# Optimization experiments

Measured on AMD Instinct MI355X. Metric: run time of the kernel, lower is better.

Reference implementation:

```python
import jax, jax.numpy as jnp
import numpy as np

B, N, H, D = 4, 2048, 16, 64
FEATS = H * D  # 1024; module scales scores by sqrt(feats), not sqrt(head_dim)


def setup_inputs() -> dict:
    key = jax.random.key(0)
    ks = jax.random.split(key, 9)
    s = 1.0 / np.sqrt(D)
    return {
        "x": jax.random.normal(ks[0], (B, N, H, D), dtype=jnp.float32),
        "Wq": jax.random.uniform(ks[1], (H, D, D), jnp.float32, -s, s),
        "bq": jax.random.uniform(ks[2], (H, D), jnp.float32, -s, s),
        "Wk": jax.random.uniform(ks[3], (H, D, D), jnp.float32, -s, s),
        "bk": jax.random.uniform(ks[4], (H, D), jnp.float32, -s, s),
        "Wv": jax.random.uniform(ks[5], (H, D, D), jnp.float32, -s, s),
        "bv": jax.random.uniform(ks[6], (H, D), jnp.float32, -s, s),
        "Wo": jax.random.uniform(ks[7], (H, D, D), jnp.float32, -s, s),
        "bo": jax.random.uniform(ks[8], (H, D), jnp.float32, -s, s),
    }


def reference(x, Wq, bq, Wk, bk, Wv, bv, Wo, bo):
    # per-head linears as one batched einsum: [b,n,h,d] x [h,d,o] -> [b,n,h,o]
    q = jnp.einsum("bnhd,hdo->bnho", x, Wq) + bq
    k = jnp.einsum("bnhd,hdo->bnho", x, Wk) + bk
    v = jnp.einsum("bnhd,hdo->bnho", x, Wv) + bv
    sqrt_d = jnp.asarray(FEATS, x.dtype) ** 0.5  # sqrt(feats) per original code
    # scores: [b,h,i,j]
    score = jax.nn.softmax(jnp.einsum("bihf,bjhf->bhij", q, k) / sqrt_d, axis=-1)
    attn = jnp.einsum("bhij,bjhf->bihf", score, v)  # [b,n,h,d]
    out = jnp.einsum("bnhd,hdo->bnho", attn, Wo) + bo
    return out
```

## Files before the change

kernel.cpp:

```cpp
#include <hip/hip_runtime.h>

#define Bsz  4
#define Nseq 2048
#define Hn   16
#define Dh   64
#define BH   (Bsz*Hn)
#define NT   (Nseq/64)

#define AS1 __attribute__((address_space(1)))
#define AS3 __attribute__((address_space(3)))

typedef __attribute__((ext_vector_type(8))) short bf16x8;
typedef __attribute__((ext_vector_type(16))) float f32x16;
typedef __attribute__((ext_vector_type(4))) float f32x4;
typedef __attribute__((ext_vector_type(2))) float f32x2;

#define MFMA32 __builtin_amdgcn_mfma_f32_32x32x16_bf16

static __device__ __forceinline__ unsigned short f2bf(float f) {
    unsigned u = __float_as_uint(f);
    u = (u + 0x7fffu + ((u >> 16) & 1u)) >> 16;
    return (unsigned short)u;
}
static __device__ __forceinline__ float bf2f(unsigned short s) {
    return __uint_as_float((unsigned)s << 16);
}
static __device__ __forceinline__ unsigned cvt_pk_bf16(float lo, float hi) {
    unsigned r;
    asm("v_cvt_pk_bf16_f32 %0, %1, %2" : "=v"(r) : "v"(lo), "v"(hi));
    return r;
}
static __device__ __forceinline__ void swap32(unsigned &a, unsigned &b) {
    asm("v_permlane32_swap_b32 %0, %1" : "+v"(a), "+v"(b));
}
static __device__ __forceinline__ float exp2v(float x) {
    float r;
    asm("v_exp_f32 %0, %1" : "=v"(r) : "v"(x));
    return r;
}
static __device__ __forceinline__ f32x2 pk_add(f32x2 a, f32x2 b) {
    f32x2 d;
    asm("v_pk_add_f32 %0, %1, %2" : "=v"(d) : "v"(a), "v"(b));
    return d;
}

__global__ __launch_bounds__(256) void proj_kernel(
    const float* __restrict__ x,
    const float* __restrict__ Wq, const float* __restrict__ bq,
    const float* __restrict__ Wk, const float* __restrict__ bk,
    const float* __restrict__ Wv, const float* __restrict__ bv,
    unsigned short* __restrict__ gQ, unsigned short* __restrict__ gK,
    unsigned short* __restrict__ gVt)
{
    const int bh = blockIdx.x, h = bh & (Hn - 1), b = bh >> 4;
    const int n0 = blockIdx.y * 64;
    const int tid = threadIdx.x;
    const int w = tid >> 6, lane = tid & 63, l31 = lane & 31, l5 = lane >> 5;
    const int qi = w >> 1, oj = w & 1;

    const int nrow = n0 + qi * 32 + l31;
    const float* xrow = x + (((size_t)b * Nseq + nrow) * Hn + h) * Dh;

    bf16x8 xh[4], xl[4];
#pragma unroll
    for (int ks = 0; ks < 4; ++ks) {
        f32x4 v0 = *(const f32x4*)&xrow[ks * 16 + l5 * 8];
        f32x4 v1 = *(const f32x4*)&xrow[ks * 16 + l5 * 8 + 4];
#pragma unroll
        for (int e = 0; e < 4; ++e) {
            unsigned short h0 = f2bf(v0[e]);
            xh[ks][e] = (short)h0;
            xl[ks][e] = (short)f2bf(v0[e] - bf2f(h0));
            unsigned short h1 = f2bf(v1[e]);
            xh[ks][4 + e] = (short)h1;
            xl[ks][4 + e] = (short)f2bf(v1[e] - bf2f(h1));
        }
    }

    const int o = oj * 32 + l31;
    const float* Wm[3] = {Wq, Wk, Wv};

    f32x16 acc[3] = {};
#pragma unroll
    for (int m = 0; m < 3; ++m) {
        const float* Wb = Wm[m] + h * 4096 + o;
#pragma unroll
        for (int ks = 0; ks < 4; ++ks) {
            bf16x8 wh, wl;
#pragma unroll
            for (int e = 0; e < 8; ++e) {
                float wv = Wb[(ks * 16 + l5 * 8 + e) * 64];
                unsigned short hh = f2bf(wv);
                wh[e] = (short)hh;
                wl[e] = (short)f2bf(wv - bf2f(hh));
            }
            if (m < 2) {
                acc[m] = MFMA32(xh[ks], wh, acc[m], 0, 0, 0);
                acc[m] = MFMA32(xl[ks], wh, acc[m], 0, 0, 0);
                acc[m] = MFMA32(xh[ks], wl, acc[m], 0, 0, 0);
            } else {
                acc[2] = MFMA32(wh, xh[ks], acc[2], 0, 0, 0);
                acc[2] = MFMA32(wl, xh[ks], acc[2], 0, 0, 0);
                acc[2] = MFMA32(wh, xl[ks], acc[2], 0, 0, 0);
            }
        }
    }

    {
        float bias = bq[h * 64 + o];
#pragma unroll
        for (int r = 0; r < 16; ++r) {
            int nl = (r & 3) + 8 * (r >> 2) + 4 * l5;
            int n = n0 + qi * 32 + nl;
            gQ[((size_t)bh * Nseq + n) * Dh + o] =
                f2bf((acc[0][r] + bias) * 0.0450842200f);
        }
    }
    {
        float bias = bk[h * 64 + o];
#pragma unroll
        for (int r = 0; r < 16; ++r) {
            int nl = (r & 3) + 8 * (r >> 2) + 4 * l5;
            int n = n0 + qi * 32 + nl;
            int c = (((o >> 3) ^ (n & 7)) * 8) + (o & 7);
            gK[((size_t)bh * Nseq + n) * Dh + c] = f2bf(acc[1][r] + bias);
        }
    }
    {
#pragma unroll
        for (int r = 0; r < 16; ++r) {
            int ol = (r & 3) + 8 * (r >> 2) + 4 * l5;
            int ov = oj * 32 + ol;
            float bias = bv[h * 64 + ov];
            int nt = qi * 32 + l31;
            int c = (((nt >> 3) ^ (ov & 7)) * 8) + (nt & 7);
            gVt[(((size_t)bh * NT + (n0 >> 6)) * 64 + ov) * 64 + c] =
                f2bf(acc[2][r] + bias);
        }
    }
}

__global__ __launch_bounds__(256, 4) void flash_kernel(
    const unsigned short* __restrict__ gQ,
    const unsigned short* __restrict__ gK,
    const unsigned short* __restrict__ gVt,
    const float* __restrict__ Wo, const float* __restrict__ bo,
    float* __restrict__ out)
{
    __shared__ unsigned short kbuf[2][4096];
    __shared__ unsigned short vbuf[2][4096];

    const int bh = blockIdx.x, h = bh & (Hn - 1), b = bh >> 4;
    const int tid = threadIdx.x;
    const int w = tid >> 6, lane = tid & 63;
    const int l31 = lane & 31, l5 = lane >> 5;
    const int qrow = blockIdx.y * 128 + w * 32 + l31;

    bf16x8 qf[4];
#pragma unroll
    for (int kk = 0; kk < 4; ++kk)
        qf[kk] = *(const bf16x8*)&gQ[((size_t)bh * Nseq + qrow) * Dh + kk * 16 + l5 * 8];

    f32x16 acc[2] = {};
    float l = 0.f;

    auto stage_kv = [&](int t, int bufi) {
        const unsigned short* ks = gK + ((size_t)bh * Nseq + (size_t)t * 64) * Dh;
        const unsigned short* vs = gVt + ((size_t)(bh * NT + t)) * 4096;
#pragma unroll
        for (int i = 0; i < 2; ++i) {
            int off = w * 1024 + i * 512 + lane * 8;
            __builtin_amdgcn_global_load_lds((const AS1 void*)(ks + off),
                                             (AS3 void*)(&kbuf[bufi][w * 1024 + i * 512]), 16, 0, 0);
            __builtin_amdgcn_global_load_lds((const AS1 void*)(vs + off),
                                             (AS3 void*)(&vbuf[bufi][w * 1024 + i * 512]), 16, 0, 0);
        }
    };

    auto tile_step = [&](const unsigned short* __restrict__ kb,
                         const unsigned short* __restrict__ vb) {
        f32x16 s[2] = {};
#pragma unroll
        for (int nt = 0; nt < 2; ++nt) {
            const int row = nt * 32 + l31;
            const int roff = row * 64;
#pragma unroll
            for (int kk = 0; kk < 4; ++kk) {
                bf16x8 kf = *(const bf16x8*)&kb[roff + (((kk * 2 + l5) ^ (row & 7)) * 8)];
                s[nt] = MFMA32(kf, qf[kk], s[nt], 0, 0, 0);
            }
        }

#pragma unroll
        for (int nt = 0; nt < 2; ++nt)
#pragma unroll
            for (int r = 0; r < 16; ++r)
                s[nt][r] = exp2v(s[nt][r]);

        f32x2* sp0 = (f32x2*)&s[0];
        f32x2* sp1 = (f32x2*)&s[1];
        f32x2 u0 = pk_add(sp0[0], sp0[1]), u1 = pk_add(sp0[2], sp0[3]);
        f32x2 u2 = pk_add(sp0[4], sp0[5]), u3 = pk_add(sp0[6], sp0[7]);
        f32x2 u4 = pk_add(sp1[0], sp1[1]), u5 = pk_add(sp1[2], sp1[3]);
        f32x2 u6 = pk_add(sp1[4], sp1[5]), u7 = pk_add(sp1[6], sp1[7]);
        u0 = pk_add(u0, u1); u2 = pk_add(u2, u3);
        u4 = pk_add(u4, u5); u6 = pk_add(u6, u7);
        u0 = pk_add(u0, u2); u4 = pk_add(u4, u6);
        u0 = pk_add(u0, u4);
        l += u0[0] + u0[1];

#pragma unroll
        for (int ks = 0; ks < 4; ++ks) {
            const int nt = ks >> 1;
            const int b0 = 8 * (ks & 1);
            unsigned x0 = cvt_pk_bf16(s[nt][b0 + 0], s[nt][b0 + 1]);
            unsigned x1 = cvt_pk_bf16(s[nt][b0 + 2], s[nt][b0 + 3]);
            unsigned y0 = cvt_pk_bf16(s[nt][b0 + 4], s[nt][b0 + 5]);
            unsigned y1 = cvt_pk_bf16(s[nt][b0 + 6], s[nt][b0 + 7]);
            swap32(x0, y0);
            swap32(x1, y1);
            bf16x8 pf;
            ((unsigned*)&pf)[0] = x0; ((unsigned*)&pf)[1] = x1;
            ((unsigned*)&pf)[2] = y0; ((unsigned*)&pf)[3] = y1;
#pragma unroll
            for (int dt = 0; dt < 2; ++dt) {
                const int row = dt * 32 + l31;
                bf16x8 vf = *(const bf16x8*)&vb[row * 64 + (((ks * 2 + l5) ^ (row & 7)) * 8)];
                acc[dt] = MFMA32(vf, pf, acc[dt], 0, 0, 0);
            }
        }
    };

    stage_kv(0, 0);

#pragma unroll 1
    for (int t2 = 0; t2 < NT; t2 += 2) {
        __syncthreads();
        stage_kv(t2 + 1, 1);
        tile_step(kbuf[0], vbuf[0]);
        __syncthreads();
        if (t2 + 2 < NT) stage_kv(t2 + 2, 0);
        tile_step(kbuf[1], vbuf[1]);
    }

    __syncthreads();
    {
        unsigned short* wl = kbuf[0];
        for (int c = tid; c < 512; c += 256) {
            int o = c >> 3, c8 = c & 7;
            int cc = ((c8 ^ (o & 7)) * 8);
#pragma unroll
            for (int jj = 0; jj < 4; ++jj) wl[o * 64 + cc + jj]     = f2bf(Wo[(h * 64 + c8 * 8 + jj) * 64 + o]);
#pragma unroll
            for (int jj = 0; jj < 4; ++jj) wl[o * 64 + cc + 4 + jj] = f2bf(Wo[(h * 64 + c8 * 8 + 4 + jj) * 64 + o]);
        }
    }
    __syncthreads();

    l += __shfl_xor(l, 32);
    float inv = 1.f / l;
#pragma unroll
    for (int dt = 0; dt < 2; ++dt)
#pragma unroll
        for (int r = 0; r < 16; ++r) acc[dt][r] *= inv;

    const unsigned short* wot = kbuf[0];
    f32x16 oc[2] = {};
#pragma unroll
    for (int kk = 0; kk < 4; ++kk) {
        const int dt = kk >> 1;
        const int b0 = 8 * (kk & 1);
        unsigned x0 = cvt_pk_bf16(acc[dt][b0 + 0], acc[dt][b0 + 1]);
        unsigned x1 = cvt_pk_bf16(acc[dt][b0 + 2], acc[dt][b0 + 3]);
        unsigned y0 = cvt_pk_bf16(acc[dt][b0 + 4], acc[dt][b0 + 5]);
        unsigned y1 = cvt_pk_bf16(acc[dt][b0 + 6], acc[dt][b0 + 7]);
        swap32(x0, y0);
        swap32(x1, y1);
        bf16x8 af;
        ((unsigned*)&af)[0] = x0; ((unsigned*)&af)[1] = x1;
        ((unsigned*)&af)[2] = y0; ((unsigned*)&af)[3] = y1;
#pragma unroll
        for (int ot = 0; ot < 2; ++ot) {
            int row = ot * 32 + l31;
            bf16x8 wf = *(const bf16x8*)&wot[row * 64 + (((kk * 2 + l5) ^ (row & 7)) * 8)];
            oc[ot] = MFMA32(wf, af, oc[ot], 0, 0, 0);
        }
    }

    float* obase = out + (((size_t)b * Nseq + qrow) * Hn + h) * Dh;
#pragma unroll
    for (int ot = 0; ot < 2; ++ot)
#pragma unroll
        for (int rq = 0; rq < 4; ++rq) {
            int o = ot * 32 + rq * 8 + l5 * 4;
            f32x4 bb = *(const f32x4*)&bo[h * 64 + o];
            f32x4 vv;
            vv[0] = oc[ot][rq * 4 + 0] + bb[0];
            vv[1] = oc[ot][rq * 4 + 1] + bb[1];
            vv[2] = oc[ot][rq * 4 + 2] + bb[2];
            vv[3] = oc[ot][rq * 4 + 3] + bb[3];
            *(f32x4*)&obase[o] = vv;
        }
}

extern "C" void kernel_launch(void* const* d_in, const int* in_sizes, int n_in,
                              void* d_out, int out_size, void* d_ws, size_t ws_size,
                              hipStream_t stream) {
    const float* x  = (const float*)d_in[0];
    const float* Wq = (const float*)d_in[1];
    const float* bq = (const float*)d_in[2];
    const float* Wk = (const float*)d_in[3];
    const float* bk = (const float*)d_in[4];
    const float* Wv = (const float*)d_in[5];
    const float* bv = (const float*)d_in[6];
    const float* Wo = (const float*)d_in[7];
    const float* bo = (const float*)d_in[8];
    float* out = (float*)d_out;

    unsigned short* gQ  = (unsigned short*)d_ws;
    unsigned short* gK  = gQ + (size_t)BH * Nseq * Dh;
    unsigned short* gVt = gK + (size_t)BH * Nseq * Dh;

    proj_kernel<<<dim3(BH, Nseq / 64), 256, 0, stream>>>(x, Wq, bq, Wk, bk, Wv, bv, gQ, gK, gVt);
    flash_kernel<<<dim3(BH, Nseq / 128), 256, 0, stream>>>(gQ, gK, gVt, Wo, bo, out);
}
```

Measured before the change: 113.9 us.

## Pre-split projection weights and software-pipeline QK with softmax-PV over 32-key tiles

Adds a small kernel that transposes Wq/Wk/Wv and splits them into bf16 hi/lo halves once, so the projection kernel loads ready bf16x8 fragments instead of doing strided fp32 loads and conversions. The flash kernel moves from 64-key tiles to 32-key tiles, with a four-slot K ring and a two-slot V ring. The QK MFMA for the next tile is issued while the exp and PV of the current tile run, aiming to overlap matrix and transcendental work. The costs are an extra kernel launch, more barriers per key, and redundant clamped loads at the end of the loop.

Result: slower. 131.1 us (+15.1%).

```diff
diff --git a/kernel.cpp b/kernel.cpp
--- a/kernel.cpp
+++ b/kernel.cpp
@@ -5,7 +5,7 @@
 #define Hn   16
 #define Dh   64
 #define BH   (Bsz*Hn)
-#define NT   (Nseq/64)
+#define NT32 (Nseq/32)
 
 #define AS1 __attribute__((address_space(1)))
 #define AS3 __attribute__((address_space(3)))
@@ -14,6 +14,7 @@
 typedef __attribute__((ext_vector_type(16))) float f32x16;
 typedef __attribute__((ext_vector_type(4))) float f32x4;
 typedef __attribute__((ext_vector_type(2))) float f32x2;
+typedef __attribute__((ext_vector_type(4))) unsigned short u16x4;
 
 #define MFMA32 __builtin_amdgcn_mfma_f32_32x32x16_bf16
 
@@ -44,11 +45,45 @@
     return d;
 }
 
+__global__ __launch_bounds__(256) void wprep_kernel(
+    const float* __restrict__ Wq, const float* __restrict__ Wk,
+    const float* __restrict__ Wv,
+    unsigned short* __restrict__ gWtH, unsigned short* __restrict__ gWtL)
+{
+    __shared__ float ws[64][65];
+    const int mh = blockIdx.x;
+    const int m = mh >> 4, h = mh & 15;
+    const int tid = threadIdx.x;
+    const float* W = (m == 0 ? Wq : (m == 1 ? Wk : Wv)) + h * 4096;
+
+    for (int c = tid; c < 1024; c += 256) {
+        int row = c >> 4, col = (c & 15) * 4;
+        *(f32x4*)&ws[row][col] = *(const f32x4*)&W[row * 64 + col];
+    }
+    __syncthreads();
+
+    const int o = tid >> 2, dblk = (tid & 3) * 16;
+    size_t base = ((size_t)mh * 64 + o) * 64 + dblk;
+#pragma unroll
+    for (int i4 = 0; i4 < 4; ++i4) {
+        u16x4 vh, vl;
+#pragma unroll
+        for (int j = 0; j < 4; ++j) {
+            float v = ws[dblk + i4 * 4 + j][o];
+            unsigned short hh = f2bf(v);
+            vh[j] = hh;
+            vl[j] = f2bf(v - bf2f(hh));
+        }
+        *(u16x4*)&gWtH[base + i4 * 4] = vh;
+        *(u16x4*)&gWtL[base + i4 * 4] = vl;
+    }
+}
+
 __global__ __launch_bounds__(256) void proj_kernel(
     const float* __restrict__ x,
-    const float* __restrict__ Wq, const float* __restrict__ bq,
-    const float* __restrict__ Wk, const float* __restrict__ bk,
-    const float* __restrict__ Wv, const float* __restrict__ bv,
+    const unsigned short* __restrict__ gWtH, const unsigned short* __restrict__ gWtL,
+    const float* __restrict__ bq, const float* __restrict__ bk,
+    const float* __restrict__ bv,
     unsigned short* __restrict__ gQ, unsigned short* __restrict__ gK,
     unsigned short* __restrict__ gVt)
 {
@@ -78,22 +113,16 @@
     }
 
     const int o = oj * 32 + l31;
-    const float* Wm[3] = {Wq, Wk, Wv};
 
     f32x16 acc[3] = {};
 #pragma unroll
     for (int m = 0; m < 3; ++m) {
-        const float* Wb = Wm[m] + h * 4096 + o;
+        const unsigned short* WH = gWtH + (((size_t)m * 16 + h) * 64 + o) * 64;
+        const unsigned short* WL = gWtL + (((size_t)m * 16 + h) * 64 + o) * 64;
 #pragma unroll
         for (int ks = 0; ks < 4; ++ks) {
-            bf16x8 wh, wl;
-#pragma unroll
-            for (int e = 0; e < 8; ++e) {
-                float wv = Wb[(ks * 16 + l5 * 8 + e) * 64];
-                unsigned short hh = f2bf(wv);
-                wh[e] = (short)hh;
-                wl[e] = (short)f2bf(wv - bf2f(hh));
-            }
+            bf16x8 wh = *(const bf16x8*)&WH[ks * 16 + l5 * 8];
+            bf16x8 wl = *(const bf16x8*)&WL[ks * 16 + l5 * 8];
             if (m < 2) {
                 acc[m] = MFMA32(xh[ks], wh, acc[m], 0, 0, 0);
                 acc[m] = MFMA32(xl[ks], wh, acc[m], 0, 0, 0);
@@ -127,14 +156,15 @@
         }
     }
     {
+        const int tile = (n0 >> 5) + qi;
+        const int kt = l31;
 #pragma unroll
         for (int r = 0; r < 16; ++r) {
             int ol = (r & 3) + 8 * (r >> 2) + 4 * l5;
             int ov = oj * 32 + ol;
             float bias = bv[h * 64 + ov];
-            int nt = qi * 32 + l31;
-            int c = (((nt >> 3) ^ (ov & 7)) * 8) + (nt & 7);
-            gVt[(((size_t)bh * NT + (n0 >> 6)) * 64 + ov) * 64 + c] =
+            int c = (((kt >> 3) ^ ((ov >> 2) & 3)) * 8) + (kt & 7);
+            gVt[(((size_t)bh * NT32 + tile) * 64 + ov) * 32 + c] =
                 f2bf(acc[2][r] + bias);
         }
     }
@@ -147,8 +177,8 @@
     const float* __restrict__ Wo, const float* __restrict__ bo,
     float* __restrict__ out)
 {
-    __shared__ unsigned short kbuf[2][4096];
-    __shared__ unsigned short vbuf[2][4096];
+    __shared__ unsigned short kbuf[4][2048];
+    __shared__ unsigned short vbuf[2][2048];
 
     const int bh = blockIdx.x, h = bh & (Hn - 1), b = bh >> 4;
     const int tid = threadIdx.x;
@@ -161,62 +191,53 @@
     for (int kk = 0; kk < 4; ++kk)
         qf[kk] = *(const bf16x8*)&gQ[((size_t)bh * Nseq + qrow) * Dh + kk * 16 + l5 * 8];
 
+    float z0 = 0.f;
+    asm volatile("" : "+v"(z0));
+    f32x16 zc = {z0, z0, z0, z0, z0, z0, z0, z0, z0, z0, z0, z0, z0, z0, z0, z0};
+
     f32x16 acc[2] = {};
     float l = 0.f;
 
-    auto stage_kv = [&](int t, int bufi) {
-        const unsigned short* ks = gK + ((size_t)bh * Nseq + (size_t)t * 64) * Dh;
-        const unsigned short* vs = gVt + ((size_t)(bh * NT + t)) * 4096;
-#pragma unroll
-        for (int i = 0; i < 2; ++i) {
-            int off = w * 1024 + i * 512 + lane * 8;
-            __builtin_amdgcn_global_load_lds((const AS1 void*)(ks + off),
-                                             (AS3 void*)(&kbuf[bufi][w * 1024 + i * 512]), 16, 0, 0);
-            __builtin_amdgcn_global_load_lds((const AS1 void*)(vs + off),
-                                             (AS3 void*)(&vbuf[bufi][w * 1024 + i * 512]), 16, 0, 0);
-        }
+    auto stageK = [&](int t, int slot) {
+        const unsigned short* src = gK + ((size_t)bh * Nseq + (size_t)t * 32) * Dh + tid * 8;
+        __builtin_amdgcn_global_load_lds((const AS1 void*)src,
+                                         (AS3 void*)(&kbuf[slot][w * 512]), 16, 0, 0);
     };
-
-    auto tile_step = [&](const unsigned short* __restrict__ kb,
-                         const unsigned short* __restrict__ vb) {
-        f32x16 s[2] = {};
-#pragma unroll
-        for (int nt = 0; nt < 2; ++nt) {
-            const int row = nt * 32 + l31;
-            const int roff = row * 64;
-#pragma unroll
-            for (int kk = 0; kk < 4; ++kk) {
-                bf16x8 kf = *(const bf16x8*)&kb[roff + (((kk * 2 + l5) ^ (row & 7)) * 8)];
-                s[nt] = MFMA32(kf, qf[kk], s[nt], 0, 0, 0);
-            }
-        }
-
-#pragma unroll
-        for (int nt = 0; nt < 2; ++nt)
-#pragma unroll
-            for (int r = 0; r < 16; ++r)
-                s[nt][r] = exp2v(s[nt][r]);
-
-        f32x2* sp0 = (f32x2*)&s[0];
-        f32x2* sp1 = (f32x2*)&s[1];
-        f32x2 u0 = pk_add(sp0[0], sp0[1]), u1 = pk_add(sp0[2], sp0[3]);
-        f32x2 u2 = pk_add(sp0[4], sp0[5]), u3 = pk_add(sp0[6], sp0[7]);
-        f32x2 u4 = pk_add(sp1[0], sp1[1]), u5 = pk_add(sp1[2], sp1[3]);
-        f32x2 u6 = pk_add(sp1[4], sp1[5]), u7 = pk_add(sp1[6], sp1[7]);
+    auto stageV = [&](int t, int slot) {
+        const unsigned short* src = gVt + ((size_t)(bh * NT32 + t)) * 2048 + tid * 8;
+        __builtin_amdgcn_global_load_lds((const AS1 void*)src,
+                                         (AS3 void*)(&vbuf[slot][w * 512]), 16, 0, 0);
+    };
+
+    auto qk_tile = [&](const unsigned short* __restrict__ kb) -> f32x16 {
+        const int roff = l31 * 64;
+        const int sw = l31 & 7;
+        bf16x8 kf = *(const bf16x8*)&kb[roff + ((l5 ^ sw) * 8)];
+        f32x16 s = MFMA32(kf, qf[0], zc, 0, 0, 0);
+#pragma unroll
+        for (int kk = 1; kk < 4; ++kk) {
+            kf = *(const bf16x8*)&kb[roff + (((kk * 2 + l5) ^ sw) * 8)];
+            s = MFMA32(kf, qf[kk], s, 0, 0, 0);
+        }
+        return s;
+    };
+
+    auto soft_pv = [&](f32x16& s, const unsigned short* __restrict__ vb) {
+#pragma unroll
+        for (int r = 0; r < 16; ++r) s[r] = exp2v(s[r]);
+        f32x2* sp = (f32x2*)&s;
+        f32x2 u0 = pk_add(sp[0], sp[1]), u1 = pk_add(sp[2], sp[3]);
+        f32x2 u2 = pk_add(sp[4], sp[5]), u3 = pk_add(sp[6], sp[7]);
         u0 = pk_add(u0, u1); u2 = pk_add(u2, u3);
-        u4 = pk_add(u4, u5); u6 = pk_add(u6, u7);
-        u0 = pk_add(u0, u2); u4 = pk_add(u4, u6);
-        u0 = pk_add(u0, u4);
+        u0 = pk_add(u0, u2);
         l += u0[0] + u0[1];
-
-#pragma unroll
-        for (int ks = 0; ks < 4; ++ks) {
-            const int nt = ks >> 1;
-            const int b0 = 8 * (ks & 1);
-            unsigned x0 = cvt_pk_bf16(s[nt][b0 + 0], s[nt][b0 + 1]);
-            unsigned x1 = cvt_pk_bf16(s[nt][b0 + 2], s[nt][b0 + 3]);
-            unsigned y0 = cvt_pk_bf16(s[nt][b0 + 4], s[nt][b0 + 5]);
-            unsigned y1 = cvt_pk_bf16(s[nt][b0 + 6], s[nt][b0 + 7]);
+#pragma unroll
+        for (int ks = 0; ks < 2; ++ks) {
+            const int b0 = 8 * ks;
+            unsigned x0 = cvt_pk_bf16(s[b0 + 0], s[b0 + 1]);
+            unsigned x1 = cvt_pk_bf16(s[b0 + 2], s[b0 + 3]);
+            unsigned y0 = cvt_pk_bf16(s[b0 + 4], s[b0 + 5]);
+            unsigned y1 = cvt_pk_bf16(s[b0 + 6], s[b0 + 7]);
             swap32(x0, y0);
             swap32(x1, y1);
             bf16x8 pf;
@@ -225,27 +246,46 @@
 #pragma unroll
             for (int dt = 0; dt < 2; ++dt) {
                 const int row = dt * 32 + l31;
-                bf16x8 vf = *(const bf16x8*)&vb[row * 64 + (((ks * 2 + l5) ^ (row & 7)) * 8)];
+                bf16x8 vf = *(const bf16x8*)&vb[row * 32 + (((ks * 2 + l5) ^ ((row >> 2) & 3)) * 8)];
                 acc[dt] = MFMA32(vf, pf, acc[dt], 0, 0, 0);
             }
         }
     };
 
-    stage_kv(0, 0);
+    stageK(0, 0);
+    stageV(0, 0);
+    stageK(1, 1);
+    __syncthreads();
+    f32x16 sA = qk_tile(kbuf[0]);
+    f32x16 sB;
 
 #pragma unroll 1
-    for (int t2 = 0; t2 < NT; t2 += 2) {
+    for (int tb = 0; tb < NT32; tb += 4) {
         __syncthreads();
-        stage_kv(t2 + 1, 1);
-        tile_step(kbuf[0], vbuf[0]);
+        stageK(min(tb + 2, NT32 - 1), 2);
+        stageV(min(tb + 1, NT32 - 1), 1);
+        sB = qk_tile(kbuf[1]);
+        soft_pv(sA, vbuf[0]);
         __syncthreads();
-        if (t2 + 2 < NT) stage_kv(t2 + 2, 0);
-        tile_step(kbuf[1], vbuf[1]);
+        stageK(min(tb + 3, NT32 - 1), 3);
+        stageV(min(tb + 2, NT32 - 1), 0);
+        sA = qk_tile(kbuf[2]);
+        soft_pv(sB, vbuf[1]);
+        __syncthreads();
+        stageK(min(tb + 4, NT32 - 1), 0);
+        stageV(min(tb + 3, NT32 - 1), 1);
+        sB = qk_tile(kbuf[3]);
+        soft_pv(sA, vbuf[0]);
+        __syncthreads();
+        stageK(min(tb + 5, NT32 - 1), 1);
+        stageV(min(tb + 4, NT32 - 1), 0);
+        sA = qk_tile(kbuf[0]);
+        soft_pv(sB, vbuf[1]);
     }
 
     __syncthreads();
     {
-        unsigned short* wl = kbuf[0];
+        unsigned short* wl = &kbuf[0][0];
         for (int c = tid; c < 512; c += 256) {
             int o = c >> 3, c8 = c & 7;
             int cc = ((c8 ^ (o & 7)) * 8);
@@ -264,7 +304,7 @@
 #pragma unroll
         for (int r = 0; r < 16; ++r) acc[dt][r] *= inv;
 
-    const unsigned short* wot = kbuf[0];
+    const unsigned short* wot = &kbuf[0][0];
     f32x16 oc[2] = {};
 #pragma unroll
     for (int kk = 0; kk < 4; ++kk) {
@@ -317,10 +357,13 @@
     const float* bo = (const float*)d_in[8];
     float* out = (float*)d_out;
 
-    unsigned short* gQ  = (unsigned short*)d_ws;
-    unsigned short* gK  = gQ + (size_t)BH * Nseq * Dh;
-    unsigned short* gVt = gK + (size_t)BH * Nseq * Dh;
-
-    proj_kernel<<<dim3(BH, Nseq / 64), 256, 0, stream>>>(x, Wq, bq, Wk, bk, Wv, bv, gQ, gK, gVt);
+    unsigned short* gQ   = (unsigned short*)d_ws;
+    unsigned short* gK   = gQ + (size_t)BH * Nseq * Dh;
+    unsigned short* gVt  = gK + (size_t)BH * Nseq * Dh;
+    unsigned short* gWtH = gVt + (size_t)BH * Nseq * Dh;
+    unsigned short* gWtL = gWtH + (size_t)3 * 16 * 64 * 64;
+
+    wprep_kernel<<<48, 256, 0, stream>>>(Wq, Wk, Wv, gWtH, gWtL);
+    proj_kernel<<<dim3(BH, Nseq / 64), 256, 0, stream>>>(x, gWtH, gWtL, bq, bk, bv, gQ, gK, gVt);
     flash_kernel<<<dim3(BH, Nseq / 128), 256, 0, stream>>>(gQ, gK, gVt, Wo, bo, out);
 }
```
